# Performance work log

Measured on AMD Instinct MI355X. Metric: run time of the kernel, lower is better.

The kernel has to match this reference:

```python
import jax, jax.numpy as jnp
import numpy as np

D_MODEL, D_K, D_V = 1024, 64, 128
NUM_HEAD = D_MODEL // D_V  # 8


def setup_inputs() -> dict:
    key = jax.random.key(0)
    ks = jax.random.split(key, 6)
    B, SQ, SKV = 4, 2048, 2048
    return {
        "encoder_output": jax.random.normal(ks[0], (B, SKV, D_MODEL), jnp.float32),
        "pre_output": jax.random.normal(ks[1], (B, SQ, D_MODEL), jnp.float32),
        "Wq": jax.random.normal(ks[2], (D_MODEL, D_K * NUM_HEAD), jnp.float32) * 0.02,
        "Wk": jax.random.normal(ks[3], (D_MODEL, D_K * NUM_HEAD), jnp.float32) * 0.02,
        "Wv": jax.random.normal(ks[4], (D_MODEL, D_MODEL), jnp.float32) * 0.02,
        "Wo": jax.random.normal(ks[5], (D_MODEL, D_MODEL), jnp.float32) * 0.02,
    }


def reference(encoder_output, pre_output, Wq, Wk, Wv, Wo):
    B, SQ, _ = pre_output.shape
    SKV = encoder_output.shape[1]
    # projections (Linear, bias=False)
    q = pre_output @ Wq          # [B, SQ, H*d_k]
    k = encoder_output @ Wk      # [B, SKV, H*d_k]
    v = encoder_output @ Wv      # [B, SKV, H*d_v] (= d_model)
    # per-head contiguous slices == reshape into head dim
    q = q.reshape(B, SQ, NUM_HEAD, D_K)
    k = k.reshape(B, SKV, NUM_HEAD, D_K)
    v = v.reshape(B, SKV, NUM_HEAD, D_V)
    scale = 1.0 / np.sqrt(D_K).astype(np.float32)
    scores = jnp.einsum("bqhd,bkhd->bhqk", q, k) * scale  # [B,H,SQ,SKV]
    attn = jax.nn.softmax(scores, axis=-1)
    out = jnp.einsum("bhqk,bkhd->bqhd", attn, v)           # [B,SQ,H,d_v]
    out = out.reshape(B, SQ, NUM_HEAD * D_V)               # concat heads
    return out @ Wo
```

## Files before the change

### kernel.cpp

```cpp
#include <hip/hip_runtime.h>
#include <math.h>

#define D_MODEL 1024
#define DK 64
#define DV 128
#define NH 8
#define BB 4
#define SQL 2048
#define SKV 2048

typedef __bf16 bf16x8 __attribute__((ext_vector_type(8)));
typedef float f32x4 __attribute__((ext_vector_type(4)));

#if __has_builtin(__builtin_amdgcn_exp2f)
#define EXP2(x) __builtin_amdgcn_exp2f(x)
#else
#define EXP2(x) exp2f(x)
#endif

#define MFMA16(a, b, c) __builtin_amdgcn_mfma_f32_16x16x32_bf16(a, b, c, 0, 0, 0)

__device__ __forceinline__ ushort f2bf(float f) {
  unsigned u = __float_as_uint(f);
  u += 0x7FFFu + ((u >> 16) & 1u);
  return (ushort)(u >> 16);
}
__device__ __forceinline__ unsigned pk2bf(float lo, float hi) {
  unsigned ul = __float_as_uint(lo);
  unsigned uh = __float_as_uint(hi);
  ul += 0x7FFFu + ((ul >> 16) & 1u);
  uh += 0x7FFFu + ((uh >> 16) & 1u);
  return __builtin_amdgcn_perm(uh, ul, 0x07060302u);
}

#define GLDS16(g, l)                                                       \
  __builtin_amdgcn_global_load_lds(                                        \
      (const __attribute__((address_space(1))) unsigned int*)(g),          \
      (__attribute__((address_space(3))) unsigned int*)(l), 16, 0, 0)

__global__ __launch_bounds__(256) void cvt2_kernel(
    const float* __restrict__ s0, const float* __restrict__ s1,
    ushort* __restrict__ d0, ushort* __restrict__ d1, int n4) {
  const float* src = blockIdx.z ? s1 : s0;
  ushort* dst = blockIdx.z ? d1 : d0;
  int i = blockIdx.x * 256 + threadIdx.x;
  if (i >= n4) return;
  float4 v = ((const float4*)src)[i];
  ushort4 o;
  o.x = f2bf(v.x); o.y = f2bf(v.y); o.z = f2bf(v.z); o.w = f2bf(v.w);
  ((ushort4*)dst)[i] = o;
}

__global__ __launch_bounds__(256) void cvt_t4_kernel(
    const float* __restrict__ W0, const float* __restrict__ W1,
    const float* __restrict__ W2, const float* __restrict__ W3,
    ushort* __restrict__ T0, ushort* __restrict__ T1, ushort* __restrict__ T2,
    ushort* __restrict__ T3) {
  __shared__ ushort T[32][34];
  const int z = blockIdx.z;
  const int C = (z < 2) ? 512 : 1024;
  const int c0 = blockIdx.y * 32;
  if (c0 >= C) return;
  const float* W = (z == 0) ? W0 : (z == 1) ? W1 : (z == 2) ? W2 : W3;
  ushort* Wt = (z == 0) ? T0 : (z == 1) ? T1 : (z == 2) ? T2 : T3;
  const int R = 1024;
  const int r0 = blockIdx.x * 32;
  const int tx = threadIdx.x, ty = threadIdx.y;
#pragma unroll
  for (int i = 0; i < 4; ++i) {
    const int rr = ty + i * 8;
    T[rr][tx] = f2bf(W[(size_t)(r0 + rr) * C + c0 + tx]);
  }
  __syncthreads();
#pragma unroll
  for (int i = 0; i < 4; ++i) {
    const int rr = ty + i * 8;
    Wt[(size_t)(c0 + rr) * R + r0 + tx] = T[tx][rr];
  }
}

__device__ __forceinline__ void gemm_core_acc(ushort (*As)[32],
                                              ushort (*Bs)[32],
                                              const ushort* At,
                                              const ushort* Bt, int K,
                                              f32x4 (&acc)[4][4]) {
  const int t = threadIdx.x;
  const int w = t >> 6, lane = t & 63;
  const int wm = (w >> 1) * 64, wn = (w & 1) * 64;
  const int lr = lane & 15, quad = lane >> 4;

  const int r0 = t >> 2;
  const int lb = (t & 3) ^ ((r0 >> 1) & 3);
  const ushort* gA0 = At + (size_t)r0 * K + lb * 8;
  const ushort* gA1 = At + (size_t)(r0 + 64) * K + lb * 8;
  const ushort* gB0 = Bt + (size_t)r0 * K + lb * 8;
  const ushort* gB1 = Bt + (size_t)(r0 + 64) * K + lb * 8;
  ushort* dA0 = (ushort*)As + t * 8;
  ushort* dA1 = (ushort*)As + t * 8 + 2048;
  ushort* dB0 = (ushort*)Bs + t * 8;
  ushort* dB1 = (ushort*)Bs + t * 8 + 2048;

  const int sw = (quad ^ ((lr >> 1) & 3)) * 8;

#pragma unroll
  for (int i = 0; i < 4; ++i)
#pragma unroll
    for (int j = 0; j < 4; ++j) acc[i][j] = (f32x4){0.f, 0.f, 0.f, 0.f};

  for (int k0 = 0; k0 < K; k0 += 32) {
    __syncthreads();
    GLDS16(gA0 + k0, dA0);
    GLDS16(gA1 + k0, dA1);
    GLDS16(gB0 + k0, dB0);
    GLDS16(gB1 + k0, dB1);
    __syncthreads();
    bf16x8 fa[4], fb[4];
#pragma unroll
    for (int i = 0; i < 4; ++i) fa[i] = *(const bf16x8*)&As[wm + i * 16 + lr][sw];
#pragma unroll
    for (int j = 0; j < 4; ++j) fb[j] = *(const bf16x8*)&Bs[wn + j * 16 + lr][sw];
#pragma unroll
    for (int i = 0; i < 4; ++i)
#pragma unroll
      for (int j = 0; j < 4; ++j) acc[i][j] = MFMA16(fa[i], fb[j], acc[i][j]);
  }
}

__global__ __launch_bounds__(256) void gemm_qkv_kernel(
    const ushort* __restrict__ preb, const ushort* __restrict__ encb,
    const ushort* __restrict__ WqkvT, ushort* __restrict__ qb,
    ushort* __restrict__ kb, ushort* __restrict__ vt, float qsc) {
  __shared__ ushort shm[17408];
  ushort(*As)[32] = (ushort(*)[32])shm;
  ushort(*Bs)[32] = (ushort(*)[32])(shm + 4096);

  const int n0 = blockIdx.x * 128, m0 = blockIdx.y * 128;
  const int t = threadIdx.x;
  const int w = t >> 6, lane = t & 63;
  const int wm = (w >> 1) * 64, wn = (w & 1) * 64;
  const int lr = lane & 15, quad = lane >> 4;

  const ushort* A = (n0 < 512) ? preb : encb;
  f32x4 acc[4][4];
  gemm_core_acc(As, Bs, A + (size_t)m0 * D_MODEL, WqkvT + (size_t)n0 * D_MODEL,
                D_MODEL, acc);

  if (n0 < 1024) {
    ushort* C = (n0 < 512) ? qb : kb;
    const int ncol = (n0 < 512) ? n0 : n0 - 512;
    const float osc = (n0 < 512) ? qsc : 1.f;
#pragma unroll
    for (int i = 0; i < 4; ++i)
#pragma unroll
      for (int j = 0; j < 4; ++j)
#pragma unroll
        for (int r = 0; r < 4; ++r) {
          const int row = m0 + wm + i * 16 + quad * 4 + r;
          const int col = ncol + wn + j * 16 + lr;
          C[(size_t)row * 512 + col] = f2bf(acc[i][j][r] * osc);
        }
  } else {
    const int h = (n0 - 1024) >> 7;
    const int b = m0 >> 11;
    const int skv0 = m0 & 2047;
    __syncthreads();
    ushort(*Ep)[68] = (ushort(*)[68])(shm + w * 4352);
#pragma unroll
    for (int i = 0; i < 4; ++i)
#pragma unroll
      for (int j = 0; j < 4; ++j) {
        uint2 dd;
        dd.x = pk2bf(acc[i][j][0], acc[i][j][1]);
        dd.y = pk2bf(acc[i][j][2], acc[i][j][3]);
        *(uint2*)&Ep[j * 16 + lr][i * 16 + quad * 4] = dd;
      }
    ushort* vbase =
        vt + ((size_t)(b * NH + h) * DV + wn) * SKV + skv0 + wm;
#pragma unroll
    for (int rep = 0; rep < 8; ++rep) {
      const int dvl = (lane >> 3) + rep * 8;
      const int skvc = (lane & 7) * 8;
      *(uint4*)&vbase[(size_t)dvl * SKV + skvc] = *(const uint4*)&Ep[dvl][skvc];
    }
  }
}

__global__ __launch_bounds__(256) void gemm_o_kernel(
    const ushort* __restrict__ ao, const ushort* __restrict__ WoT,
    float* __restrict__ out) {
  __shared__ ushort As[128][32];
  __shared__ ushort Bs[128][32];
  const int n0 = blockIdx.x * 128, m0 = blockIdx.y * 128;
  const int t = threadIdx.x;
  const int w = t >> 6, lane = t & 63;
  const int wm = (w >> 1) * 64, wn = (w & 1) * 64;
  const int lr = lane & 15, quad = lane >> 4;
  f32x4 acc[4][4];
  gemm_core_acc(As, Bs, ao + (size_t)m0 * D_MODEL, WoT + (size_t)n0 * D_MODEL,
                D_MODEL, acc);
#pragma unroll
  for (int i = 0; i < 4; ++i)
#pragma unroll
    for (int j = 0; j < 4; ++j)
#pragma unroll
      for (int r = 0; r < 4; ++r) {
        const int row = m0 + wm + i * 16 + quad * 4 + r;
        const int col = n0 + wn + j * 16 + lr;
        out[(size_t)row * D_MODEL + col] = acc[i][j][r];
      }
}

__global__ __launch_bounds__(256) void attn_mfma_kernel(
    const ushort* __restrict__ Q, const ushort* __restrict__ Kb,
    const ushort* __restrict__ Vt, ushort* __restrict__ Oo) {
  __shared__ ushort Ks[128][64];
  __shared__ ushort Vs[128][128];
  __shared__ ushort Ps[4][32][36];

  const int t = threadIdx.x;
  const int qt = blockIdx.x, h = blockIdx.y, b = blockIdx.z;
  const int w = t >> 6, lane = t & 63;
  const int lr = lane & 15, quad = lane >> 4;
  const int q0 = qt * 128 + w * 32;

  union { bf16x8 v; ushort u[8]; } one8;
#pragma unroll
  for (int i = 0; i < 8; ++i) one8.u[i] = 0x3F80;

  bf16x8 aq[2][2];
#pragma unroll
  for (int mt = 0; mt < 2; ++mt)
#pragma unroll
    for (int kh = 0; kh < 2; ++kh)
      aq[mt][kh] = *(const bf16x8*)&Q[(size_t)(b * SQL + q0 + mt * 16 + lr) *
                                          (NH * DK) +
                                      h * DK + kh * 32 + quad * 8];

  f32x4 accO[2][9];
#pragma unroll
  for (int mt = 0; mt < 2; ++mt)
#pragma unroll
    for (int dn = 0; dn < 9; ++dn) accO[mt][dn] = (f32x4){0.f, 0.f, 0.f, 0.f};

  const ushort* kbase = Kb + (size_t)b * SKV * (NH * DK) + h * DK;
  const ushort* vbase = Vt + (size_t)(b * NH + h) * DV * SKV;

  const int krow = t >> 3;
  const int kblk = (t & 7) ^ (krow & 7);
  const ushort* gK = kbase + (size_t)krow * (NH * DK) + kblk * 8;
  ushort* dK = (ushort*)Ks + t * 8;
  const int vrow = t >> 4;
  const int vkv = ((t & 15) ^ (vrow & 15)) * 8;
  const ushort* gV = vbase + (size_t)vrow * SKV + vkv;
  ushort* dV = (ushort*)Vs + t * 8;

  const int swk = lr & 7;

  for (int kv0 = 0; kv0 < SKV; kv0 += 128) {
    __syncthreads();
#pragma unroll
    for (int rd = 0; rd < 4; ++rd)
      GLDS16(gK + (size_t)(kv0 + rd * 32) * (NH * DK), dK + rd * 2048);
#pragma unroll
    for (int rd = 0; rd < 8; ++rd)
      GLDS16(gV + (size_t)rd * 16 * SKV + kv0, dV + rd * 2048);
    __syncthreads();

#pragma unroll
    for (int c = 0; c < 4; ++c) {
#pragma unroll
      for (int tt = 0; tt < 2; ++tt) {
        const int nt = c * 2 + tt;
        const bf16x8 fk0 = *(const bf16x8*)&Ks[nt * 16 + lr][(quad ^ swk) * 8];
        const bf16x8 fk1 =
            *(const bf16x8*)&Ks[nt * 16 + lr][((4 + quad) ^ swk) * 8];
#pragma unroll
        for (int mt = 0; mt < 2; ++mt) {
          f32x4 s = (f32x4){0.f, 0.f, 0.f, 0.f};
          s = MFMA16(fk0, aq[mt][0], s);
          s = MFMA16(fk1, aq[mt][1], s);
          const unsigned u0 = __float_as_uint(EXP2(s[0]));
          const unsigned u1 = __float_as_uint(EXP2(s[1]));
          const unsigned u2 = __float_as_uint(EXP2(s[2]));
          const unsigned u3 = __float_as_uint(EXP2(s[3]));
          uint2 dd;
          dd.x = __builtin_amdgcn_perm(u1, u0, 0x07060302u);
          dd.y = __builtin_amdgcn_perm(u3, u2, 0x07060302u);
          *(uint2*)&Ps[w][mt * 16 + lr][tt * 16 + quad * 4] = dd;
        }
      }
      bf16x8 ap[2];
#pragma unroll
      for (int mt = 0; mt < 2; ++mt) {
        union { bf16x8 v; uint2 u[2]; } fr;
        fr.u[0] = *(const uint2*)&Ps[w][mt * 16 + lr][quad * 8];
        fr.u[1] = *(const uint2*)&Ps[w][mt * 16 + lr][quad * 8 + 4];
        ap[mt] = fr.v;
      }
#pragma unroll
      for (int dn = 0; dn < 8; ++dn) {
        const bf16x8 fv =
            *(const bf16x8*)&Vs[dn * 16 + lr][((c * 4 + quad) ^ lr) * 8];
        accO[0][dn] = MFMA16(ap[0], fv, accO[0][dn]);
        accO[1][dn] = MFMA16(ap[1], fv, accO[1][dn]);
      }
      accO[0][8] = MFMA16(ap[0], one8.v, accO[0][8]);
      accO[1][8] = MFMA16(ap[1], one8.v, accO[1][8]);
    }
  }

#pragma unroll
  for (int mt = 0; mt < 2; ++mt) {
    float inv[4];
#pragma unroll
    for (int r = 0; r < 4; ++r) inv[r] = 1.f / accO[mt][8][r];
#pragma unroll
    for (int dn = 0; dn < 8; ++dn)
#pragma unroll
      for (int r = 0; r < 4; ++r) {
        const size_t row = (size_t)b * SQL + q0 + mt * 16 + quad * 4 + r;
        Oo[row * D_MODEL + h * DV + dn * 16 + lr] =
            f2bf(accO[mt][dn][r] * inv[r]);
      }
  }
}

extern "C" void kernel_launch(void* const* d_in, const int* in_sizes, int n_in,
                              void* d_out, int out_size, void* d_ws,
                              size_t ws_size, hipStream_t stream) {
  const float* enc = (const float*)d_in[0];
  const float* pre = (const float*)d_in[1];
  const float* Wq = (const float*)d_in[2];
  const float* Wk = (const float*)d_in[3];
  const float* Wv = (const float*)d_in[4];
  const float* Wo = (const float*)d_in[5];
  float* out = (float*)d_out;

  const int M = BB * SQL;

  ushort* encb = (ushort*)d_ws;
  ushort* preb = encb + (size_t)M * D_MODEL;
  ushort* WqT = preb + (size_t)M * D_MODEL;
  ushort* WkT = WqT + (size_t)(NH * DK) * D_MODEL;
  ushort* WvT = WkT + (size_t)(NH * DK) * D_MODEL;
  ushort* WoT = WvT + (size_t)D_MODEL * D_MODEL;
  ushort* qb = WoT + (size_t)D_MODEL * D_MODEL;
  ushort* kb = qb + (size_t)M * (NH * DK);
  ushort* vt = kb + (size_t)M * (NH * DK);
  ushort* ao = encb;

  const int n4 = M * D_MODEL / 4;
  dim3 blk(256);
  dim3 tblk(32, 8);

  cvt2_kernel<<<dim3(n4 / 256, 1, 2), blk, 0, stream>>>(enc, pre, encb, preb,
                                                        n4);
  cvt_t4_kernel<<<dim3(32, 32, 4), tblk, 0, stream>>>(Wq, Wk, Wv, Wo, WqT, WkT,
                                                      WvT, WoT);

  gemm_qkv_kernel<<<dim3(16, 64), blk, 0, stream>>>(
      preb, encb, WqT, qb, kb, vt, 0.18033688011112042f);

  attn_mfma_kernel<<<dim3(SQL / 128, NH, BB), blk, 0, stream>>>(qb, kb, vt, ao);

  gemm_o_kernel<<<dim3(8, 64), blk, 0, stream>>>(ao, WoT, out);
}
```

Measured before the change: 285.1 us.

## Double-buffer K/V tiles in attention kernel with async prefetch and block swizzle

```diff
diff --git a/kernel.cpp b/kernel.cpp
--- a/kernel.cpp
+++ b/kernel.cpp
@@ -213,15 +213,19 @@
 __global__ __launch_bounds__(256) void attn_mfma_kernel(
     const ushort* __restrict__ Q, const ushort* __restrict__ Kb,
     const ushort* __restrict__ Vt, ushort* __restrict__ Oo) {
-  __shared__ ushort Ks[128][64];
-  __shared__ ushort Vs[128][128];
+  __shared__ ushort Ks[2][64][64];
+  __shared__ ushort Vs[2][128][64];
   __shared__ ushort Ps[4][32][36];
 
   const int t = threadIdx.x;
-  const int qt = blockIdx.x, h = blockIdx.y, b = blockIdx.z;
+  const int n = blockIdx.x + 16 * blockIdx.y + 128 * blockIdx.z;
+  const int l = (n & 7) * 64 + (n >> 3);
+  const int qt = l & 15, h = (l >> 4) & 7, b = l >> 7;
+
   const int w = t >> 6, lane = t & 63;
   const int lr = lane & 15, quad = lane >> 4;
   const int q0 = qt * 128 + w * 32;
+  const int swk = lr & 7;
 
   union { bf16x8 v; ushort u[8]; } one8;
 #pragma unroll
@@ -245,69 +249,87 @@
   const ushort* kbase = Kb + (size_t)b * SKV * (NH * DK) + h * DK;
   const ushort* vbase = Vt + (size_t)(b * NH + h) * DV * SKV;
 
-  const int krow = t >> 3;
-  const int kblk = (t & 7) ^ (krow & 7);
-  const ushort* gK = kbase + (size_t)krow * (NH * DK) + kblk * 8;
+  const int srow = t >> 3;
+  const int sb7 = (t & 7) ^ (srow & 7);
+  const ushort* gK = kbase + (size_t)srow * (NH * DK) + sb7 * 8;
+  const ushort* gV = vbase + (size_t)srow * SKV + sb7 * 8;
   ushort* dK = (ushort*)Ks + t * 8;
-  const int vrow = t >> 4;
-  const int vkv = ((t & 15) ^ (vrow & 15)) * 8;
-  const ushort* gV = vbase + (size_t)vrow * SKV + vkv;
   ushort* dV = (ushort*)Vs + t * 8;
 
-  const int swk = lr & 7;
-
-  for (int kv0 = 0; kv0 < SKV; kv0 += 128) {
-    __syncthreads();
-#pragma unroll
-    for (int rd = 0; rd < 4; ++rd)
-      GLDS16(gK + (size_t)(kv0 + rd * 32) * (NH * DK), dK + rd * 2048);
-#pragma unroll
-    for (int rd = 0; rd < 8; ++rd)
-      GLDS16(gV + (size_t)rd * 16 * SKV + kv0, dV + rd * 2048);
-    __syncthreads();
-
-#pragma unroll
-    for (int c = 0; c < 4; ++c) {
-#pragma unroll
-      for (int tt = 0; tt < 2; ++tt) {
-        const int nt = c * 2 + tt;
-        const bf16x8 fk0 = *(const bf16x8*)&Ks[nt * 16 + lr][(quad ^ swk) * 8];
-        const bf16x8 fk1 =
-            *(const bf16x8*)&Ks[nt * 16 + lr][((4 + quad) ^ swk) * 8];
-#pragma unroll
-        for (int mt = 0; mt < 2; ++mt) {
-          f32x4 s = (f32x4){0.f, 0.f, 0.f, 0.f};
-          s = MFMA16(fk0, aq[mt][0], s);
-          s = MFMA16(fk1, aq[mt][1], s);
-          const unsigned u0 = __float_as_uint(EXP2(s[0]));
-          const unsigned u1 = __float_as_uint(EXP2(s[1]));
-          const unsigned u2 = __float_as_uint(EXP2(s[2]));
-          const unsigned u3 = __float_as_uint(EXP2(s[3]));
-          uint2 dd;
-          dd.x = __builtin_amdgcn_perm(u1, u0, 0x07060302u);
-          dd.y = __builtin_amdgcn_perm(u3, u2, 0x07060302u);
-          *(uint2*)&Ps[w][mt * 16 + lr][tt * 16 + quad * 4] = dd;
-        }
+  auto stage = [&](int kv0, int buf) {
+    const ushort* gk = gK + (size_t)kv0 * (NH * DK);
+    ushort* dk = dK + buf * 4096;
+    GLDS16(gk, dk);
+    GLDS16(gk + (size_t)32 * (NH * DK), dk + 2048);
+    const ushort* gv = gV + kv0;
+    ushort* dv = dV + buf * 8192;
+    GLDS16(gv, dv);
+    GLDS16(gv + (size_t)32 * SKV, dv + 2048);
+    GLDS16(gv + (size_t)64 * SKV, dv + 4096);
+    GLDS16(gv + (size_t)96 * SKV, dv + 6144);
+  };
+
+  auto chunk = [&](const ushort(*Kc)[64], const ushort(*Vc)[64], int c) {
+#pragma unroll
+    for (int tt = 0; tt < 2; ++tt) {
+      const int nt = c * 2 + tt;
+      const bf16x8 fk0 = *(const bf16x8*)&Kc[nt * 16 + lr][(quad ^ swk) * 8];
+      const bf16x8 fk1 =
+          *(const bf16x8*)&Kc[nt * 16 + lr][((4 + quad) ^ swk) * 8];
+#pragma unroll
+      for (int mt = 0; mt < 2; ++mt) {
+        f32x4 s = (f32x4){0.f, 0.f, 0.f, 0.f};
+        s = MFMA16(fk0, aq[mt][0], s);
+        s = MFMA16(fk1, aq[mt][1], s);
+        const unsigned u0 = __float_as_uint(EXP2(s[0]));
+        const unsigned u1 = __float_as_uint(EXP2(s[1]));
+        const unsigned u2 = __float_as_uint(EXP2(s[2]));
+        const unsigned u3 = __float_as_uint(EXP2(s[3]));
+        uint2 dd;
+        dd.x = __builtin_amdgcn_perm(u1, u0, 0x07060302u);
+        dd.y = __builtin_amdgcn_perm(u3, u2, 0x07060302u);
+        *(uint2*)&Ps[w][mt * 16 + lr][tt * 16 + quad * 4] = dd;
       }
-      bf16x8 ap[2];
-#pragma unroll
-      for (int mt = 0; mt < 2; ++mt) {
-        union { bf16x8 v; uint2 u[2]; } fr;
-        fr.u[0] = *(const uint2*)&Ps[w][mt * 16 + lr][quad * 8];
-        fr.u[1] = *(const uint2*)&Ps[w][mt * 16 + lr][quad * 8 + 4];
-        ap[mt] = fr.v;
-      }
-#pragma unroll
-      for (int dn = 0; dn < 8; ++dn) {
-        const bf16x8 fv =
-            *(const bf16x8*)&Vs[dn * 16 + lr][((c * 4 + quad) ^ lr) * 8];
-        accO[0][dn] = MFMA16(ap[0], fv, accO[0][dn]);
-        accO[1][dn] = MFMA16(ap[1], fv, accO[1][dn]);
-      }
-      accO[0][8] = MFMA16(ap[0], one8.v, accO[0][8]);
-      accO[1][8] = MFMA16(ap[1], one8.v, accO[1][8]);
     }
-  }
+    bf16x8 ap[2];
+#pragma unroll
+    for (int mt = 0; mt < 2; ++mt) {
+      union { bf16x8 v; uint2 u[2]; } fr;
+      fr.u[0] = *(const uint2*)&Ps[w][mt * 16 + lr][quad * 8];
+      fr.u[1] = *(const uint2*)&Ps[w][mt * 16 + lr][quad * 8 + 4];
+      ap[mt] = fr.v;
+    }
+    __builtin_amdgcn_s_setprio(1);
+#pragma unroll
+    for (int dn = 0; dn < 8; ++dn) {
+      const bf16x8 fv =
+          *(const bf16x8*)&Vc[dn * 16 + lr][((c * 4 + quad) ^ swk) * 8];
+      accO[0][dn] = MFMA16(ap[0], fv, accO[0][dn]);
+      accO[1][dn] = MFMA16(ap[1], fv, accO[1][dn]);
+    }
+    accO[0][8] = MFMA16(ap[0], one8.v, accO[0][8]);
+    accO[1][8] = MFMA16(ap[1], one8.v, accO[1][8]);
+    __builtin_amdgcn_s_setprio(0);
+  };
+
+  stage(0, 0);
+  for (int ti = 0; ti < 31; ++ti) {
+    stage((ti + 1) * 64, (ti + 1) & 1);
+    asm volatile("s_waitcnt vmcnt(6)" ::: "memory");
+    __builtin_amdgcn_s_barrier();
+    __builtin_amdgcn_sched_barrier(0);
+    const ushort(*Kc)[64] = Ks[ti & 1];
+    const ushort(*Vc)[64] = Vs[ti & 1];
+    chunk(Kc, Vc, 0);
+    chunk(Kc, Vc, 1);
+    __builtin_amdgcn_sched_barrier(0);
+    __builtin_amdgcn_s_barrier();
+  }
+  asm volatile("s_waitcnt vmcnt(0)" ::: "memory");
+  __builtin_amdgcn_s_barrier();
+  __builtin_amdgcn_sched_barrier(0);
+  chunk(Ks[1], Vs[1], 0);
+  chunk(Ks[1], Vs[1], 1);
 
 #pragma unroll
   for (int mt = 0; mt < 2; ++mt) {
```

Measured after the change: 264.5 us. -7.2%, faster.
